# Optimization experiments

Hardware: AMD Instinct MI355X
Metric: run time of the kernel (lower is better)

Reference implementation:

```python
import jax, jax.numpy as jnp
import numpy as np
from jax import lax

B, ROWS, COLS, K, LATENT = 8, 1536, 16, 32, 16
EPS_REG = 0.01  # torchsort regularization_strength
BIG = 1e30


def setup_inputs() -> dict:
    key = jax.random.key(0)
    ks = jax.random.split(key, 12)
    def w(k, shape):
        return (jax.random.normal(k, shape, jnp.float32) / np.sqrt(shape[0])).astype(jnp.float32)
    return {
        "table": jax.random.uniform(ks[0], (B, ROWS, COLS), jnp.float32),
        "enc_w1": w(ks[1], (COLS, 32)), "enc_b1": 0.01 * jax.random.normal(ks[2], (32,), jnp.float32),
        "enc_w2": w(ks[3], (32, 64)),   "enc_b2": 0.01 * jax.random.normal(ks[4], (64,), jnp.float32),
        "mean_w": w(ks[5], (64, LATENT)), "mean_b": 0.01 * jax.random.normal(ks[6], (LATENT,), jnp.float32),
        "dec_w1": w(ks[7], (LATENT, 32)), "dec_b1": 0.01 * jax.random.normal(ks[8], (32,), jnp.float32),
        "dec_w2": w(ks[9], (32, COLS)),   "dec_b2": 0.01 * jax.random.normal(ks[10], (COLS,), jnp.float32),
        "labels": jax.random.randint(ks[11], (ROWS,), 0, K, jnp.int32),
        "BlockSize": 64,
        "current_epoch": 0,
        "baseline": 0,
    }


def _soft_rank_l2(s, eps):
    # Exact soft_rank (Blondel et al. / torchsort, l2 reg, ascending):
    # project s/eps onto permutahedron of (n,...,1).
    n = s.shape[0]
    x = s / eps
    perm = jnp.argsort(-x)            # descending sort
    xs = x[perm]
    w = jnp.arange(n, 0, -1, dtype=x.dtype)
    # dual = non-increasing isotonic fit of y = xs - w == -iso_inc(-(xs - w))
    y = -(xs - w)
    S = jnp.concatenate([jnp.zeros((1,), x.dtype), jnp.cumsum(y)])
    idx = jnp.arange(n)
    length = jnp.maximum(idx[None, :] - idx[:, None] + 1, 1).astype(x.dtype)
    A = (S[1:][None, :] - S[:n][:, None]) / length           # mean(y[j..k])  [j,k]
    A = jnp.where(idx[None, :] >= idx[:, None], A, BIG)
    Bm = lax.cummin(A, axis=1, reverse=True)                  # min_{k>=i} A[j,k]
    Cm = lax.cummax(Bm, axis=0)                               # max_{j<=i} ...
    iso_inc = jnp.diagonal(Cm)
    dual = -iso_inc
    primal = xs - dual
    inv = jnp.argsort(perm)
    return primal[inv]


def _forward(table, enc_w1, enc_b1, enc_w2, enc_b2, mean_w, mean_b,
             dec_w1, dec_b1, dec_w2, dec_b2, labels, BlockSize):
    b = table.shape[0]
    # VAE (autoencoder path; z = latent mean)
    h = jax.nn.relu(table @ enc_w1 + enc_b1)
    h = jax.nn.relu(h @ enc_w2 + enc_b2)
    z = h @ mean_w + mean_b                                   # [B, rows, 16]
    r = jax.nn.relu(z @ dec_w1 + dec_b1)
    recon = jax.nn.relu(r @ dec_w2 + dec_b2)
    loss = jnp.mean((recon - table) ** 2)
    # clustering scores (labels fixed from batch 0, shared across batch)
    onehot = jax.nn.one_hot(labels, K, dtype=z.dtype)         # [rows, K]
    counts = jnp.maximum(onehot.sum(0), 1.0)                  # [K]
    centers = jnp.einsum('brd,rk->bkd', z, onehot) / counts[None, :, None]
    center_data = centers[:, labels, :]                       # gather back [B, rows, 16]
    d2 = jnp.mean((z - center_data) ** 2, axis=-1)            # [B, rows]
    mn = d2.min(axis=1, keepdims=True); mx = d2.max(axis=1, keepdims=True)
    d2 = (d2 - mn) / (mx - mn)
    scores = d2 + labels.astype(z.dtype)[None, :]
    # training branch
    smn = scores.min(axis=1, keepdims=True); smx = scores.max(axis=1, keepdims=True)
    scaled = (scores - smn) / (smx - smn) * jnp.asarray(b, z.dtype)  # * len(table)
    ranks = jax.vmap(lambda s: _soft_rank_l2(s, EPS_REG))(scaled)
    rank_idx = jnp.argsort(jnp.argsort(scores, axis=1), axis=1) // BlockSize + 1
    rows = table.shape[1]
    return (ranks.reshape(b, rows, 1), rank_idx.reshape(b, rows, 1),
            scores.reshape(b, rows, 1), loss)


def reference(table, enc_w1, enc_b1, enc_w2, enc_b2, mean_w, mean_b,
              dec_w1, dec_b1, dec_w2, dec_b2, labels, BlockSize,
              current_epoch, baseline):
    return _forward(table, enc_w1, enc_b1, enc_w2, enc_b2, mean_w, mean_b,
                    dec_w1, dec_b1, dec_w2, dec_b2, labels, BlockSize)
```

## Files before the change

kernel.cpp:

```cpp
#include <hip/hip_runtime.h>

#define BATCH 8
#define ROWS 1536
#define KCLS 32
#define NTOT (BATCH*ROWS)
#define ELEMS (NTOT*16)
#define SSTRIDE 3073
#define BIGF 1.0e30f

enum : int {
  WS_Z     = 0,
  WS_XS    = WS_Z + NTOT*16,
  WS_S     = WS_XS + NTOT,
  WS_DESC  = WS_S + BATCH*SSTRIDE,
  WS_ASCP  = WS_DESC + NTOT,
  WS_DSCP  = WS_ASCP + 4*NTOT,
  WS_GPART = WS_DSCP + 4*NTOT,
  WS_LOSSP = WS_GPART + BATCH*96*512,
  WS_D2    = WS_LOSSP + 768,
  WS_MM    = WS_D2 + NTOT,
  WS_CPAR2 = WS_MM + 96,
  WS_CNT   = WS_CPAR2 + BATCH*8*512,
};
#define WS_CPART WS_GPART

#define LW1  0
#define LB1  512
#define LW2  544
#define LB2  2592
#define LMW  2656
#define LMB  3680
#define LDW1 3696
#define LDB1 4208
#define LDW2 4240
#define LDB2 4752
#define LTOT 4768

#define AX   0
#define AH1  16
#define AH2  48
#define AZ   112
#define AR1  128
#define AREC 144
#define ASTRIDE 164

#define RPB 16

template<int IN_BASE, int IN_N, int OUT_BASE, int OUT_PW, int OUT_TOT,
         int WOFF, int BOFF, bool RELU>
__device__ __forceinline__ void layerw(float* __restrict__ act,
                                       const float* __restrict__ wsh,
                                       int lrow, int fway)
{
  const int o0 = fway * OUT_PW;
  float a0[OUT_PW], a1[OUT_PW], a2[OUT_PW], a3[OUT_PW];
#pragma unroll
  for (int j = 0; j < OUT_PW; ++j) {
    a0[j] = wsh[BOFF + o0 + j];
    a1[j] = 0.f; a2[j] = 0.f; a3[j] = 0.f;
  }

  const float4* arow = reinterpret_cast<const float4*>(&act[lrow*ASTRIDE + IN_BASE]);
#pragma unroll
  for (int i4 = 0; i4 < IN_N/4; ++i4) {
    const float4 sv = arow[i4];
    const float* wp0 = &wsh[WOFF + (i4*4 + 0)*OUT_TOT + o0];
    const float* wp1 = &wsh[WOFF + (i4*4 + 1)*OUT_TOT + o0];
    const float* wp2 = &wsh[WOFF + (i4*4 + 2)*OUT_TOT + o0];
    const float* wp3 = &wsh[WOFF + (i4*4 + 3)*OUT_TOT + o0];
    if constexpr (OUT_PW == 1) {
      a0[0] = fmaf(sv.x, wp0[0], a0[0]);
      a1[0] = fmaf(sv.y, wp1[0], a1[0]);
      a2[0] = fmaf(sv.z, wp2[0], a2[0]);
      a3[0] = fmaf(sv.w, wp3[0], a3[0]);
    } else if constexpr (OUT_PW == 2) {
      const float2 w0 = *reinterpret_cast<const float2*>(wp0);
      const float2 w1 = *reinterpret_cast<const float2*>(wp1);
      const float2 w2 = *reinterpret_cast<const float2*>(wp2);
      const float2 w3 = *reinterpret_cast<const float2*>(wp3);
      a0[0] = fmaf(sv.x, w0.x, a0[0]); a0[1] = fmaf(sv.x, w0.y, a0[1]);
      a1[0] = fmaf(sv.y, w1.x, a1[0]); a1[1] = fmaf(sv.y, w1.y, a1[1]);
      a2[0] = fmaf(sv.z, w2.x, a2[0]); a2[1] = fmaf(sv.z, w2.y, a2[1]);
      a3[0] = fmaf(sv.w, w3.x, a3[0]); a3[1] = fmaf(sv.w, w3.y, a3[1]);
    } else {
#pragma unroll
      for (int q = 0; q < OUT_PW/4; ++q) {
        const float4 w0 = reinterpret_cast<const float4*>(wp0)[q];
        const float4 w1 = reinterpret_cast<const float4*>(wp1)[q];
        const float4 w2 = reinterpret_cast<const float4*>(wp2)[q];
        const float4 w3 = reinterpret_cast<const float4*>(wp3)[q];
        a0[q*4+0] = fmaf(sv.x, w0.x, a0[q*4+0]);
        a0[q*4+1] = fmaf(sv.x, w0.y, a0[q*4+1]);
        a0[q*4+2] = fmaf(sv.x, w0.z, a0[q*4+2]);
        a0[q*4+3] = fmaf(sv.x, w0.w, a0[q*4+3]);
        a1[q*4+0] = fmaf(sv.y, w1.x, a1[q*4+0]);
        a1[q*4+1] = fmaf(sv.y, w1.y, a1[q*4+1]);
        a1[q*4+2] = fmaf(sv.y, w1.z, a1[q*4+2]);
        a1[q*4+3] = fmaf(sv.y, w1.w, a1[q*4+3]);
        a2[q*4+0] = fmaf(sv.z, w2.x, a2[q*4+0]);
        a2[q*4+1] = fmaf(sv.z, w2.y, a2[q*4+1]);
        a2[q*4+2] = fmaf(sv.z, w2.z, a2[q*4+2]);
        a2[q*4+3] = fmaf(sv.z, w2.w, a2[q*4+3]);
        a3[q*4+0] = fmaf(sv.w, w3.x, a3[q*4+0]);
        a3[q*4+1] = fmaf(sv.w, w3.y, a3[q*4+1]);
        a3[q*4+2] = fmaf(sv.w, w3.z, a3[q*4+2]);
        a3[q*4+3] = fmaf(sv.w, w3.w, a3[q*4+3]);
      }
    }
  }

  float* orow = &act[lrow*ASTRIDE + OUT_BASE + o0];
  if constexpr (OUT_PW == 1) {
    float v = (a0[0] + a1[0]) + (a2[0] + a3[0]);
    orow[0] = RELU ? fmaxf(v, 0.f) : v;
  } else if constexpr (OUT_PW == 2) {
    float2 v;
    v.x = (a0[0] + a1[0]) + (a2[0] + a3[0]);
    v.y = (a0[1] + a1[1]) + (a2[1] + a3[1]);
    if (RELU) { v.x = fmaxf(v.x, 0.f); v.y = fmaxf(v.y, 0.f); }
    *reinterpret_cast<float2*>(orow) = v;
  } else {
#pragma unroll
    for (int q = 0; q < OUT_PW/4; ++q) {
      float4 v;
      v.x = (a0[q*4+0] + a1[q*4+0]) + (a2[q*4+0] + a3[q*4+0]);
      v.y = (a0[q*4+1] + a1[q*4+1]) + (a2[q*4+1] + a3[q*4+1]);
      v.z = (a0[q*4+2] + a1[q*4+2]) + (a2[q*4+2] + a3[q*4+2]);
      v.w = (a0[q*4+3] + a1[q*4+3]) + (a2[q*4+3] + a3[q*4+3]);
      if (RELU) {
        v.x = fmaxf(v.x, 0.f); v.y = fmaxf(v.y, 0.f);
        v.z = fmaxf(v.z, 0.f); v.w = fmaxf(v.w, 0.f);
      }
      reinterpret_cast<float4*>(orow)[q] = v;
    }
  }
}

__global__ __launch_bounds__(256, 4) void k1_ae(
    const float* __restrict__ table,
    const float* __restrict__ w1, const float* __restrict__ b1,
    const float* __restrict__ w2, const float* __restrict__ b2,
    const float* __restrict__ mw, const float* __restrict__ mb,
    const float* __restrict__ dw1, const float* __restrict__ db1,
    const float* __restrict__ dw2, const float* __restrict__ db2,
    const int* __restrict__ labels,
    float* __restrict__ ws)
{
  const int tid  = threadIdx.x;
  const int lrow = tid & (RPB-1);
  const int fway = tid >> 4;
  const int blk  = blockIdx.x;
  const int b    = blk / 96;
  const int ch   = blk % 96;

  __shared__ float wsh[LTOT];
  __shared__ float act[RPB * ASTRIDE];
  __shared__ int   lbl[RPB];
  __shared__ float lred[4];

  {
    float4* d4 = reinterpret_cast<float4*>(wsh);
#define CPY(off, src, nf4) \
    { const float4* p = reinterpret_cast<const float4*>(src); \
      for (int t = tid; t < (nf4); t += 256) d4[(off)/4 + t] = p[t]; }
    CPY(LW1,  w1,  128) CPY(LB1,  b1,  8)  CPY(LW2,  w2,  512)
    CPY(LB2,  b2,  16)  CPY(LMW,  mw,  256) CPY(LMB,  mb,  4)
    CPY(LDW1, dw1, 128) CPY(LDB1, db1, 8)  CPY(LDW2, dw2, 128)
    CPY(LDB2, db2, 4)
#undef CPY
    if (tid < RPB) lbl[tid] = labels[ch * RPB + tid];
    if (tid < RPB*4) {
      const float4 v = reinterpret_cast<const float4*>(table)[blk*(RPB*4) + tid];
      reinterpret_cast<float4*>(act)[(tid >> 2)*(ASTRIDE/4) + (tid & 3)] = v;
    }
  }
  __syncthreads();

  layerw<AX,  16, AH1, 2, 32, LW1,  LB1,  true >(act, wsh, lrow, fway);
  __syncthreads();
  layerw<AH1, 32, AH2, 4, 64, LW2,  LB2,  true >(act, wsh, lrow, fway);
  __syncthreads();
  layerw<AH2, 64, AZ,  1, 16, LMW,  LMB,  false>(act, wsh, lrow, fway);
  __syncthreads();

  if (tid < RPB*4) {
    const float4 zv =
      reinterpret_cast<const float4*>(act)[(tid >> 2)*(ASTRIDE/4) + (AZ/4) + (tid & 3)];
    reinterpret_cast<float4*>(ws + WS_Z)[blk*(RPB*4) + tid] = zv;
  }

  layerw<AZ,  16, AR1, 2, 32, LDW1, LDB1, true >(act, wsh, lrow, fway);
  __syncthreads();
  layerw<AR1, 32, AREC,1, 16, LDW2, LDB2, true >(act, wsh, lrow, fway);
  __syncthreads();

  {
    const float d = act[lrow*ASTRIDE + AREC + fway] - act[lrow*ASTRIDE + AX + fway];
    float ls = d * d;
    for (int off = 32; off > 0; off >>= 1) ls += __shfl_down(ls, off);
    if ((tid & 63) == 0) lred[tid >> 6] = ls;
    __syncthreads();
    if (tid == 0) ws[WS_LOSSP + blk] = (lred[0] + lred[1]) + (lred[2] + lred[3]);
  }

  {
    float a0 = 0.f, a1 = 0.f;
    const int d0 = tid & 15, k0 = tid >> 4;
    const int k1c = k0 + 16;
#pragma unroll
    for (int rr = 0; rr < RPB; ++rr) {
      const int lb = lbl[rr];
      const float zv = act[rr*ASTRIDE + AZ + d0];
      a0 += (lb == k0)  ? zv : 0.f;
      a1 += (lb == k1c) ? zv : 0.f;
    }
    ws[WS_CPART + (b*96 + ch)*512 + tid]       = a0;
    ws[WS_CPART + (b*96 + ch)*512 + 256 + tid] = a1;
  }
}

__global__ __launch_bounds__(512) void kcen(const int* __restrict__ labels,
                                            float* __restrict__ ws,
                                            float* __restrict__ out)
{
  const int bi = blockIdx.x;
  const int b = bi >> 3, g = bi & 7;
  const int tid = threadIdx.x;

  const float* cp = ws + WS_CPART + (b*96 + g*12)*512 + tid;
  float s = 0.f;
#pragma unroll
  for (int c = 0; c < 12; ++c) s += cp[c*512];
  ws[WS_CPAR2 + (b*8 + g)*512 + tid] = s;

  if (bi == 0) {
    __shared__ int icnt[KCLS];
    __shared__ float red[512];
    if (tid < KCLS) icnt[tid] = 0;
    __syncthreads();
    atomicAdd(&icnt[labels[tid]], 1);
    atomicAdd(&icnt[labels[512 + tid]], 1);
    atomicAdd(&icnt[labels[1024 + tid]], 1);
    red[tid] = ws[WS_LOSSP + tid] + ((tid < 256) ? ws[WS_LOSSP + 512 + tid] : 0.f);
    __syncthreads();
    for (int off = 256; off > 0; off >>= 1) {
      if (tid < off) red[tid] += red[tid + off];
      __syncthreads();
    }
    if (tid == 0) out[3*NTOT] = red[0] / (float)ELEMS;
    if (tid < KCLS) reinterpret_cast<int*>(ws)[WS_CNT + tid] = icnt[tid];
  }
}

__global__ __launch_bounds__(256) void kd2(const int* __restrict__ labels,
                                           float* __restrict__ ws)
{
  const int bi = blockIdx.x;
  const int b = bi / 6, ib = bi % 6;
  const int tid = threadIdx.x;

  __shared__ float cent[512];
  __shared__ float rmn[256], rmx[256];
  __shared__ int ci[KCLS];

  if (tid < KCLS) ci[tid] = reinterpret_cast<const int*>(ws)[WS_CNT + tid];
  float s1 = 0.f, s2 = 0.f;
#pragma unroll
  for (int g = 0; g < 8; ++g) {
    s1 += ws[WS_CPAR2 + (b*8 + g)*512 + tid];
    s2 += ws[WS_CPAR2 + (b*8 + g)*512 + 256 + tid];
  }
  __syncthreads();
  {
    int cn1 = ci[tid >> 4];         cn1 = cn1 > 1 ? cn1 : 1;
    int cn2 = ci[(tid + 256) >> 4]; cn2 = cn2 > 1 ? cn2 : 1;
    cent[tid]       = s1 / (float)cn1;
    cent[tid + 256] = s2 / (float)cn2;
  }
  __syncthreads();

  const int r = ib*256 + tid;
  const int lb = labels[r];
  const float4* zp = reinterpret_cast<const float4*>(ws + WS_Z + (b*ROWS + r)*16);
  const float4* cq = reinterpret_cast<const float4*>(&cent[lb*16]);
  float s = 0.f;
#pragma unroll
  for (int q = 0; q < 4; ++q) {
    float4 zv = zp[q], cv = cq[q];
    float d0 = zv.x - cv.x, d1 = zv.y - cv.y, d2_ = zv.z - cv.z, d3 = zv.w - cv.w;
    s += d0*d0 + d1*d1 + d2_*d2_ + d3*d3;
  }
  const float dv = s / 16.f;
  ws[WS_D2 + b*ROWS + r] = dv;
  rmn[tid] = dv; rmx[tid] = dv;
  __syncthreads();
  for (int off = 128; off > 0; off >>= 1) {
    if (tid < off) {
      rmn[tid] = fminf(rmn[tid], rmn[tid + off]);
      rmx[tid] = fmaxf(rmx[tid], rmx[tid + off]);
    }
    __syncthreads();
  }
  if (tid == 0) {
    ws[WS_MM + bi*2]     = rmn[0];
    ws[WS_MM + bi*2 + 1] = rmx[0];
  }
}

__global__ __launch_bounds__(256) void kcount(const int* __restrict__ labels,
                                              float* __restrict__ ws,
                                              float* __restrict__ out)
{
  const int bi = blockIdx.x;
  const int jb = bi & 3, rb = (bi >> 2) % 6, b = bi / 24;
  const int tid = threadIdx.x;

  alignas(16) __shared__ float s_l[ROWS];

  float mn = 3.0e38f, mx = -3.0e38f;
#pragma unroll
  for (int c = 0; c < 6; ++c) {
    mn = fminf(mn, ws[WS_MM + (b*6 + c)*2]);
    mx = fmaxf(mx, ws[WS_MM + (b*6 + c)*2 + 1]);
  }

#pragma unroll
  for (int c = 0; c < 6; ++c) {
    const int r = c*256 + tid;
    const float sc = (ws[WS_D2 + b*ROWS + r] - mn) / (mx - mn) + (float)labels[r];
    s_l[r] = sc;
    if (jb == 0 && c == rb) out[2*NTOT + b*ROWS + r] = sc;
  }
  __syncthreads();

  const int r0 = rb*256 + tid;
  const float si = s_l[r0];
  int asc = 0, dsc = 0;
  const int j0 = jb*384;
  const float4* s4p = reinterpret_cast<const float4*>(&s_l[j0]);
#pragma unroll 4
  for (int kk = 0; kk < 96; ++kk) {
    const float4 s4 = s4p[kk];
    const int j = j0 + kk*4;
    const bool t0 = (s4.x == si && j   < r0);
    const bool t1 = (s4.y == si && j+1 < r0);
    const bool t2 = (s4.z == si && j+2 < r0);
    const bool t3 = (s4.w == si && j+3 < r0);
    asc += (s4.x < si || t0) ? 1 : 0;
    asc += (s4.y < si || t1) ? 1 : 0;
    asc += (s4.z < si || t2) ? 1 : 0;
    asc += (s4.w < si || t3) ? 1 : 0;
    dsc += (s4.x > si || t0) ? 1 : 0;
    dsc += (s4.y > si || t1) ? 1 : 0;
    dsc += (s4.z > si || t2) ? 1 : 0;
    dsc += (s4.w > si || t3) ? 1 : 0;
  }
  int* wsi = reinterpret_cast<int*>(ws);
  wsi[WS_ASCP + jb*NTOT + b*ROWS + r0] = asc;
  wsi[WS_DSCP + jb*NTOT + b*ROWS + r0] = dsc;
}

__global__ __launch_bounds__(256) void k67(const int* __restrict__ bsp,
                                           float* __restrict__ ws,
                                           float* __restrict__ out)
{
  const int b = blockIdx.x, tid = threadIdx.x;
  const int lane = tid & 63, wav = tid >> 6;
  __shared__ float xs_l[ROWS];
  __shared__ float rmn[256], rmx[256];
  __shared__ float wtot[4];
  const int* wsi = reinterpret_cast<const int*>(ws);
  int* wsw = reinterpret_cast<int*>(ws);
  const int BS = *bsp;

  int dscv[6];
  float sv[6];
  float tmn = 3.0e38f, tmx = -3.0e38f;
#pragma unroll
  for (int c = 0; c < 6; ++c) {
    const int r = c*256 + tid;
    const int idx = b*ROWS + r;
    int asc = 0, dsc = 0;
#pragma unroll
    for (int jb = 0; jb < 4; ++jb) {
      asc += wsi[WS_ASCP + jb*NTOT + idx];
      dsc += wsi[WS_DSCP + jb*NTOT + idx];
    }
    out[NTOT + idx] = (float)(asc / BS + 1);
    wsw[WS_DESC + idx] = dsc;
    dscv[c] = dsc;
    const float sc = out[2*NTOT + idx];
    sv[c] = sc;
    tmn = fminf(tmn, sc); tmx = fmaxf(tmx, sc);
  }
  rmn[tid] = tmn; rmx[tid] = tmx;
  __syncthreads();
  for (int off = 128; off > 0; off >>= 1) {
    if (tid < off) {
      rmn[tid] = fminf(rmn[tid], rmn[tid + off]);
      rmx[tid] = fmaxf(rmx[tid], rmx[tid + off]);
    }
    __syncthreads();
  }
  const float smn = rmn[0], smx = rmx[0];
  __syncthreads();

#pragma unroll
  for (int c = 0; c < 6; ++c) {
    const float scl = (sv[c] - smn) / (smx - smn) * 8.0f;
    xs_l[dscv[c]] = scl / 0.01f;
  }
  __syncthreads();

  const int base = tid * 6;
  float y[6], own = 0.f;
#pragma unroll
  for (int u = 0; u < 6; ++u) {
    ws[WS_XS + b*ROWS + base + u] = xs_l[base + u];
    y[u] = (float)(ROWS - (base + u)) - xs_l[base + u];
    own += y[u];
  }
  float v = own;
#pragma unroll
  for (int d = 1; d < 64; d <<= 1) {
    float o = __shfl_up(v, d);
    if (lane >= d) v += o;
  }
  if (lane == 63) wtot[wav] = v;
  __syncthreads();
  float wpre = 0.f;
  for (int w = 0; w < wav; ++w) wpre += wtot[w];
  float run = wpre + (v - own);
  float* S = ws + WS_S + b*SSTRIDE;
#pragma unroll
  for (int u = 0; u < 6; ++u) { S[base + u] = run; run += y[u]; }
  if (tid == 255) S[ROWS] = run;
#pragma unroll
  for (int u = 0; u < 6; ++u) S[ROWS + 1 + tid*6 + u] = BIGF;
}

__global__ __launch_bounds__(256) void k8a(float* __restrict__ ws)
{
  const int bi = blockIdx.x;
  const int c = bi & 7, ib = (bi >> 3) % 6, b = bi / 48;
  const int tid = threadIdx.x;
  __shared__ float Sseg[448];
  __shared__ float invl[192];
  const float* S = ws + WS_S + b*SSTRIDE;
  const int ibase = ib*256;
  const int segbase = ibase + c*192 + 1;
  Sseg[tid] = S[segbase + tid];
  if (tid < 192) {
    Sseg[256 + tid] = S[segbase + 256 + tid];
    invl[tid] = 1.0f / (float)(c*192 + tid + 1);
  }
  __syncthreads();
  const int i = ibase + tid;
  const float Si = S[i];
  float gm = 3.0e38f;
#pragma unroll 8
  for (int k = 0; k < 192; ++k)
    gm = fminf(gm, (Sseg[tid + k] - Si) * invl[k]);
  ws[WS_GPART + (b*8 + c)*ROWS + i] = gm;
}

__global__ __launch_bounds__(768) void k8b(float* __restrict__ ws,
                                           float* __restrict__ out)
{
  const int b = blockIdx.x, tid = threadIdx.x;
  const int lane = tid & 63, wav = tid >> 6;
  __shared__ float g[ROWS];
  __shared__ float wtot[12];
  for (int t = tid; t < ROWS; t += 768) {
    float gm = 3.0e38f;
#pragma unroll
    for (int c = 0; c < 8; ++c)
      gm = fminf(gm, ws[WS_GPART + (b*8 + c)*ROWS + t]);
    g[t] = gm;
  }
  __syncthreads();
  const float a = g[2*tid], cc = g[2*tid + 1];
  float v = fmaxf(a, cc);
#pragma unroll
  for (int d = 1; d < 64; d <<= 1) {
    float o = __shfl_up(v, d);
    if (lane >= d) v = fmaxf(v, o);
  }
  if (lane == 63) wtot[wav] = v;
  __syncthreads();
  float wpre = -3.0e38f;
  for (int w = 0; w < wav; ++w) wpre = fmaxf(wpre, wtot[w]);
  float lex = __shfl_up(v, 1);
  if (lane == 0) lex = -3.0e38f;
  const float excl = fmaxf(wpre, lex);
  const float i0 = fmaxf(excl, a);
  const float i1 = fmaxf(i0, cc);
  g[2*tid] = i0; g[2*tid + 1] = i1;
  __syncthreads();
  const float* xs = ws + WS_XS + b*ROWS;
  const int* desc = reinterpret_cast<const int*>(ws) + WS_DESC + b*ROWS;
  for (int t = tid; t < ROWS; t += 768) {
    const int dr = desc[t];
    out[b*ROWS + t] = xs[dr] + g[dr];
  }
}

extern "C" void kernel_launch(void* const* d_in, const int* in_sizes, int n_in,
                              void* d_out, int out_size, void* d_ws, size_t ws_size,
                              hipStream_t stream) {
  const float* table = (const float*)d_in[0];
  const float* w1  = (const float*)d_in[1];
  const float* b1  = (const float*)d_in[2];
  const float* w2  = (const float*)d_in[3];
  const float* b2  = (const float*)d_in[4];
  const float* mw  = (const float*)d_in[5];
  const float* mb  = (const float*)d_in[6];
  const float* dw1 = (const float*)d_in[7];
  const float* db1 = (const float*)d_in[8];
  const float* dw2 = (const float*)d_in[9];
  const float* db2 = (const float*)d_in[10];
  const int* labels = (const int*)d_in[11];
  const int* bsp    = (const int*)d_in[12];
  float* out = (float*)d_out;
  float* ws  = (float*)d_ws;

  k1_ae<<<768, 256, 0, stream>>>(table, w1, b1, w2, b2, mw, mb, dw1, db1, dw2, db2, labels, ws);
  kcen<<<64, 512, 0, stream>>>(labels, ws, out);
  kd2<<<48, 256, 0, stream>>>(labels, ws);
  kcount<<<192, 256, 0, stream>>>(labels, ws, out);
  k67<<<8, 256, 0, stream>>>(bsp, ws, out);
  k8a<<<384, 256, 0, stream>>>(ws);
  k8b<<<8, 768, 0, stream>>>(ws, out);
}
```

Baseline: 59.36 us.

## Fuse center, distance and min/max kernels into counting kernel

Removes the kcen and kd2 launches and has each kcount block redundantly reduce the 96 center partials, count labels, compute the per-row distances and the batch min/max itself, and block 0 also reduces the loss. This cuts two kernel launches and their global round trips. In exchange, each of the 192 blocks repeats the full per-batch centroid and distance work (24x redundancy), which adds memory reads and latency inside the counting kernel.

```diff
diff --git a/kernel.cpp b/kernel.cpp
--- a/kernel.cpp
+++ b/kernel.cpp
@@ -17,10 +17,6 @@
   WS_DSCP  = WS_ASCP + 4*NTOT,
   WS_GPART = WS_DSCP + 4*NTOT,
   WS_LOSSP = WS_GPART + BATCH*96*512,
-  WS_D2    = WS_LOSSP + 768,
-  WS_MM    = WS_D2 + NTOT,
-  WS_CPAR2 = WS_MM + 96,
-  WS_CNT   = WS_CPAR2 + BATCH*8*512,
 };
 #define WS_CPART WS_GPART
 
@@ -219,94 +215,6 @@
   }
 }
 
-__global__ __launch_bounds__(512) void kcen(const int* __restrict__ labels,
-                                            float* __restrict__ ws,
-                                            float* __restrict__ out)
-{
-  const int bi = blockIdx.x;
-  const int b = bi >> 3, g = bi & 7;
-  const int tid = threadIdx.x;
-
-  const float* cp = ws + WS_CPART + (b*96 + g*12)*512 + tid;
-  float s = 0.f;
-#pragma unroll
-  for (int c = 0; c < 12; ++c) s += cp[c*512];
-  ws[WS_CPAR2 + (b*8 + g)*512 + tid] = s;
-
-  if (bi == 0) {
-    __shared__ int icnt[KCLS];
-    __shared__ float red[512];
-    if (tid < KCLS) icnt[tid] = 0;
-    __syncthreads();
-    atomicAdd(&icnt[labels[tid]], 1);
-    atomicAdd(&icnt[labels[512 + tid]], 1);
-    atomicAdd(&icnt[labels[1024 + tid]], 1);
-    red[tid] = ws[WS_LOSSP + tid] + ((tid < 256) ? ws[WS_LOSSP + 512 + tid] : 0.f);
-    __syncthreads();
-    for (int off = 256; off > 0; off >>= 1) {
-      if (tid < off) red[tid] += red[tid + off];
-      __syncthreads();
-    }
-    if (tid == 0) out[3*NTOT] = red[0] / (float)ELEMS;
-    if (tid < KCLS) reinterpret_cast<int*>(ws)[WS_CNT + tid] = icnt[tid];
-  }
-}
-
-__global__ __launch_bounds__(256) void kd2(const int* __restrict__ labels,
-                                           float* __restrict__ ws)
-{
-  const int bi = blockIdx.x;
-  const int b = bi / 6, ib = bi % 6;
-  const int tid = threadIdx.x;
-
-  __shared__ float cent[512];
-  __shared__ float rmn[256], rmx[256];
-  __shared__ int ci[KCLS];
-
-  if (tid < KCLS) ci[tid] = reinterpret_cast<const int*>(ws)[WS_CNT + tid];
-  float s1 = 0.f, s2 = 0.f;
-#pragma unroll
-  for (int g = 0; g < 8; ++g) {
-    s1 += ws[WS_CPAR2 + (b*8 + g)*512 + tid];
-    s2 += ws[WS_CPAR2 + (b*8 + g)*512 + 256 + tid];
-  }
-  __syncthreads();
-  {
-    int cn1 = ci[tid >> 4];         cn1 = cn1 > 1 ? cn1 : 1;
-    int cn2 = ci[(tid + 256) >> 4]; cn2 = cn2 > 1 ? cn2 : 1;
-    cent[tid]       = s1 / (float)cn1;
-    cent[tid + 256] = s2 / (float)cn2;
-  }
-  __syncthreads();
-
-  const int r = ib*256 + tid;
-  const int lb = labels[r];
-  const float4* zp = reinterpret_cast<const float4*>(ws + WS_Z + (b*ROWS + r)*16);
-  const float4* cq = reinterpret_cast<const float4*>(&cent[lb*16]);
-  float s = 0.f;
-#pragma unroll
-  for (int q = 0; q < 4; ++q) {
-    float4 zv = zp[q], cv = cq[q];
-    float d0 = zv.x - cv.x, d1 = zv.y - cv.y, d2_ = zv.z - cv.z, d3 = zv.w - cv.w;
-    s += d0*d0 + d1*d1 + d2_*d2_ + d3*d3;
-  }
-  const float dv = s / 16.f;
-  ws[WS_D2 + b*ROWS + r] = dv;
-  rmn[tid] = dv; rmx[tid] = dv;
-  __syncthreads();
-  for (int off = 128; off > 0; off >>= 1) {
-    if (tid < off) {
-      rmn[tid] = fminf(rmn[tid], rmn[tid + off]);
-      rmx[tid] = fmaxf(rmx[tid], rmx[tid + off]);
-    }
-    __syncthreads();
-  }
-  if (tid == 0) {
-    ws[WS_MM + bi*2]     = rmn[0];
-    ws[WS_MM + bi*2 + 1] = rmx[0];
-  }
-}
-
 __global__ __launch_bounds__(256) void kcount(const int* __restrict__ labels,
                                               float* __restrict__ ws,
                                               float* __restrict__ out)
@@ -316,18 +224,72 @@
   const int tid = threadIdx.x;
 
   alignas(16) __shared__ float s_l[ROWS];
-
-  float mn = 3.0e38f, mx = -3.0e38f;
+  __shared__ float cent[512];
+  __shared__ float rmn[256], rmx[256];
+  __shared__ int cnt[KCLS];
+
+  if (tid < KCLS) cnt[tid] = 0;
+  __syncthreads();
+
+  int lbv[6];
 #pragma unroll
   for (int c = 0; c < 6; ++c) {
-    mn = fminf(mn, ws[WS_MM + (b*6 + c)*2]);
-    mx = fmaxf(mx, ws[WS_MM + (b*6 + c)*2 + 1]);
-  }
-
+    lbv[c] = labels[c*256 + tid];
+    atomicAdd(&cnt[lbv[c]], 1);
+  }
+
+  float s1a = 0.f, s1b = 0.f, s2a = 0.f, s2b = 0.f;
+  {
+    const float* cp = ws + WS_CPART + (b*96)*512;
+#pragma unroll 4
+    for (int c = 0; c < 96; c += 2) {
+      s1a += cp[c*512 + tid];
+      s1b += cp[(c+1)*512 + tid];
+      s2a += cp[c*512 + 256 + tid];
+      s2b += cp[(c+1)*512 + 256 + tid];
+    }
+  }
+  __syncthreads();
+  {
+    int cn1 = cnt[tid >> 4];         cn1 = cn1 > 1 ? cn1 : 1;
+    int cn2 = cnt[(tid + 256) >> 4]; cn2 = cn2 > 1 ? cn2 : 1;
+    cent[tid]       = (s1a + s1b) / (float)cn1;
+    cent[tid + 256] = (s2a + s2b) / (float)cn2;
+  }
+  __syncthreads();
+
+  float dv[6];
+  float tmn = 3.0e38f, tmx = -3.0e38f;
 #pragma unroll
   for (int c = 0; c < 6; ++c) {
     const int r = c*256 + tid;
-    const float sc = (ws[WS_D2 + b*ROWS + r] - mn) / (mx - mn) + (float)labels[r];
+    const float4* zp = reinterpret_cast<const float4*>(ws + WS_Z + (b*ROWS + r)*16);
+    const float4* cq = reinterpret_cast<const float4*>(&cent[lbv[c]*16]);
+    float s = 0.f;
+#pragma unroll
+    for (int q = 0; q < 4; ++q) {
+      float4 zv = zp[q], cv = cq[q];
+      float d0 = zv.x - cv.x, d1 = zv.y - cv.y, d2_ = zv.z - cv.z, d3 = zv.w - cv.w;
+      s += d0*d0 + d1*d1 + d2_*d2_ + d3*d3;
+    }
+    dv[c] = s / 16.f;
+    tmn = fminf(tmn, dv[c]); tmx = fmaxf(tmx, dv[c]);
+  }
+  rmn[tid] = tmn; rmx[tid] = tmx;
+  __syncthreads();
+  for (int off = 128; off > 0; off >>= 1) {
+    if (tid < off) {
+      rmn[tid] = fminf(rmn[tid], rmn[tid + off]);
+      rmx[tid] = fmaxf(rmx[tid], rmx[tid + off]);
+    }
+    __syncthreads();
+  }
+  const float mn = rmn[0], mx = rmx[0];
+
+#pragma unroll
+  for (int c = 0; c < 6; ++c) {
+    const int r = c*256 + tid;
+    const float sc = (dv[c] - mn) / (mx - mn) + (float)lbv[c];
     s_l[r] = sc;
     if (jb == 0 && c == rb) out[2*NTOT + b*ROWS + r] = sc;
   }
@@ -358,6 +320,17 @@
   int* wsi = reinterpret_cast<int*>(ws);
   wsi[WS_ASCP + jb*NTOT + b*ROWS + r0] = asc;
   wsi[WS_DSCP + jb*NTOT + b*ROWS + r0] = dsc;
+
+  if (bi == 0) {
+    __syncthreads();
+    rmn[tid] = ws[WS_LOSSP + tid] + ws[WS_LOSSP + 256 + tid] + ws[WS_LOSSP + 512 + tid];
+    __syncthreads();
+    for (int off = 128; off > 0; off >>= 1) {
+      if (tid < off) rmn[tid] += rmn[tid + off];
+      __syncthreads();
+    }
+    if (tid == 0) out[3*NTOT] = rmn[0] / (float)ELEMS;
+  }
 }
 
 __global__ __launch_bounds__(256) void k67(const int* __restrict__ bsp,
@@ -525,8 +498,6 @@
   float* ws  = (float*)d_ws;
 
   k1_ae<<<768, 256, 0, stream>>>(table, w1, b1, w2, b2, mw, mb, dw1, db1, dw2, db2, labels, ws);
-  kcen<<<64, 512, 0, stream>>>(labels, ws, out);
-  kd2<<<48, 256, 0, stream>>>(labels, ws);
   kcount<<<192, 256, 0, stream>>>(labels, ws, out);
   k67<<<8, 256, 0, stream>>>(bsp, ws, out);
   k8a<<<384, 256, 0, stream>>>(ws);
```

After: 62.01 us. +4.5%, slower.
